# Performance work log

Measured on AMD Instinct MI355X. Metric: run time of the kernel, lower is better.

Reference implementation:

```python
import jax, jax.numpy as jnp
import numpy as np

NUM_HEADS = 12

def _rotate_half(t):
    t1, t2 = jnp.split(t, 2, axis=-1)
    return jnp.concatenate([-t2, t1], axis=-1)

def _rope_apply(t, sin, cos):
    # t: [B,H,N,Dh]; sin/cos: [N,Dh] broadcast over B,H
    return t * cos + _rotate_half(t) * sin


def setup_inputs() -> dict:
    key = jax.random.key(0)
    ks = jax.random.split(key, 6)
    B, N, D = 2, 2048, 768
    Dh = D // NUM_HEADS
    return {
        "x": jax.random.normal(ks[0], (B, N, D), dtype=jnp.float32),
        "sin": jax.random.uniform(ks[1], (N, Dh), dtype=jnp.float32),
        "cos": jax.random.uniform(ks[2], (N, Dh), dtype=jnp.float32),
        "qkv_w": jax.random.normal(ks[3], (3 * D, D), dtype=jnp.float32) * (D ** -0.5),
        "proj_w": jax.random.normal(ks[4], (D, D), dtype=jnp.float32) * (D ** -0.5),
        "proj_b": jax.random.normal(ks[5], (D,), dtype=jnp.float32),
    }


def reference(x, sin, cos, qkv_w, proj_w, proj_b):
    B, N, D = x.shape
    H = NUM_HEADS
    Dh = D // H
    scale = Dh ** -0.5
    # fused QKV projection (qkv_bias=False)
    qkv = jnp.einsum("bnd,ed->bne", x, qkv_w)              # [B,N,3D]
    qkv = qkv.reshape(B, N, 3, H, Dh)
    q = jnp.transpose(qkv[:, :, 0], (0, 2, 1, 3))          # [B,H,N,Dh]
    k = jnp.transpose(qkv[:, :, 1], (0, 2, 1, 3))
    v = jnp.transpose(qkv[:, :, 2], (0, 2, 1, 3))
    # inline RoPE (prefix = 0: sin/cos cover all N positions)
    q = _rope_apply(q, sin, cos)
    k = _rope_apply(k, sin, cos)
    # scaled dot-product attention
    scores = jnp.einsum("bhqd,bhkd->bhqk", q, k) * scale   # [B,H,N,N]
    attn = jax.nn.softmax(scores, axis=-1)
    out = jnp.einsum("bhqk,bhkd->bhqd", attn, v)           # [B,H,N,Dh]
    out = jnp.transpose(out, (0, 2, 1, 3)).reshape(B, N, D)
    # output projection
    return jnp.einsum("bnd,ed->bne", out, proj_w) + proj_b
```

## Files before the change

### kernel.cpp

```cpp
#include <hip/hip_runtime.h>
#include <hip/hip_bf16.h>
#include <stdint.h>


typedef unsigned short u16;
typedef __attribute__((ext_vector_type(8))) short s16x8;
typedef __attribute__((ext_vector_type(4))) short s16x4;
typedef __attribute__((ext_vector_type(4))) float f32x4;

#define MFMA16(a, b, c) __builtin_amdgcn_mfma_f32_16x16x32_bf16((a), (b), (c), 0, 0, 0)

__device__ __forceinline__ f32x4 mfma_k16(s16x4 a, s16x4 b, f32x4 c) {
    asm("s_nop 3\n\tv_mfma_f32_16x16x16_bf16 %0, %1, %2, %0"
        : "+v"(c) : "v"(a), "v"(b));
    return c;
}

__device__ __forceinline__ u16 f2bf(float f) {
    uint32_t u = __float_as_uint(f);
    u = u + 0x7fffu + ((u >> 16) & 1u);
    return (u16)(u >> 16);
}
__device__ __forceinline__ uint32_t pk2(float lo, float hi) {
    return (uint32_t)f2bf(lo) | ((uint32_t)f2bf(hi) << 16);
}
__device__ __forceinline__ uint32_t pk2t(float lo, float hi) {
    return __builtin_amdgcn_perm(__float_as_uint(hi), __float_as_uint(lo),
                                 0x07060302u);
}
__device__ __forceinline__ float fexp2(float x) { return __builtin_amdgcn_exp2f(x); }

__device__ __forceinline__ void gload16(const void* g, void* l) {
    __builtin_amdgcn_global_load_lds(
        (const __attribute__((address_space(1))) unsigned int*)g,
        (__attribute__((address_space(3))) unsigned int*)l,
        16, 0, 0);
}

__global__ __launch_bounds__(256)
void k_cvt3(const float* __restrict__ s0, const float* __restrict__ s1,
            const float* __restrict__ s2, u16* __restrict__ dst,
            int a, int ab, int tot)
{
    const int i = blockIdx.x * 256 + threadIdx.x;
    if (i >= tot) return;
    const float4* src;
    if (i < a)       src = (const float4*)s0 + i;
    else if (i < ab) src = (const float4*)s1 + (i - a);
    else             src = (const float4*)s2 + (i - ab);
    const float4 v = *src;
    ushort4 o;
    o.x = f2bf(v.x); o.y = f2bf(v.y); o.z = f2bf(v.z); o.w = f2bf(v.w);
    ((ushort4*)dst)[i] = o;
}

__global__ __launch_bounds__(256, 2)
void k_qkv_rope(const u16* __restrict__ X,
                const u16* __restrict__ W,
                const float* __restrict__ SIN,
                const float* __restrict__ COS,
                u16* __restrict__ qws, u16* __restrict__ kws, u16* __restrict__ vtws)
{
    __shared__ u16 smem[17408];
    u16* const As0 = smem;
    u16* const Bs0 = smem + 8192;

    const int t  = threadIdx.x;
    const int l  = t & 63;
    const int w  = t >> 6;
    const int cl = l & 15, gh = l >> 4;
    const int brow = blockIdx.x * 128;
    const int bcol = blockIdx.y * 128;
    const int wr = (w >> 1) * 64;
    const int wc = (w & 1) * 64;

    const int srow = w * 16 + (l >> 2);
    const int scol = (((l & 3) ^ ((l >> 3) & 3)) * 8);
    const u16* gA = X + (size_t)(brow + srow) * 768 + scol;
    const u16* gB = W + (size_t)(bcol + srow) * 768 + scol;

    const int csw = ((cl >> 1) & 3);

    f32x4 acc[4][4] = {};

    gload16(gA,            As0 + w * 512);
    gload16(gA + 64 * 768, As0 + 2048 + w * 512);
    gload16(gB,            Bs0 + w * 512);
    gload16(gB + 64 * 768, Bs0 + 2048 + w * 512);
    __syncthreads();

    for (int kt = 0; kt < 24; ++kt) {
        const int cur = kt & 1;
        if (kt + 1 < 24) {
            const int k0 = (kt + 1) * 32;
            u16* An = As0 + (cur ^ 1) * 4096;
            u16* Bn = Bs0 + (cur ^ 1) * 4096;
            gload16(gA + k0,            An + w * 512);
            gload16(gA + k0 + 64 * 768, An + 2048 + w * 512);
            gload16(gB + k0,            Bn + w * 512);
            gload16(gB + k0 + 64 * 768, Bn + 2048 + w * 512);
        }
        const char* Ac = (const char*)(As0 + cur * 4096);
        const char* Bc = (const char*)(Bs0 + cur * 4096);
        s16x8 af[4], bv[4];
        #pragma unroll
        for (int m = 0; m < 4; ++m) {
            const int row = wr + m * 16 + cl;
            af[m] = *(const s16x8*)(Ac + row * 64 + ((gh ^ csw) << 4));
        }
        #pragma unroll
        for (int n = 0; n < 4; ++n) {
            const int row = wc + n * 16 + cl;
            bv[n] = *(const s16x8*)(Bc + row * 64 + ((gh ^ csw) << 4));
        }
        #pragma unroll
        for (int m = 0; m < 4; ++m)
            #pragma unroll
            for (int n = 0; n < 4; ++n)
                acc[m][n] = MFMA16(af[m], bv[n], acc[m][n]);
        __syncthreads();
    }

    if (blockIdx.y >= 12) {
        u16* const Vt = smem;
        #pragma unroll
        for (int m = 0; m < 4; ++m)
            #pragma unroll
            for (int jj = 0; jj < 4; ++jj) {
                const int rowl = wr + m * 16 + gh * 4 + jj;
                #pragma unroll
                for (int n = 0; n < 4; ++n)
                    Vt[(wc + n * 16 + cl) * 136 + rowl] = f2bf(acc[m][n][jj]);
            }
        __syncthreads();
        const int dhcol = t >> 1;
        const int c     = t & 1;
        const int gcol  = bcol + dhcol;
        const int h     = (gcol >> 6) - 24;
        const int dh    = gcol & 63;
        const int b     = brow >> 11;
        const int tok0  = (brow & 2047) + c * 64;
        u16* dst = vtws + ((size_t)(b * 12 + h) * 64 + dh) * 2048 + tok0;
        const uint4* src = (const uint4*)((const char*)Vt + dhcol * 272 + c * 128);
        #pragma unroll
        for (int j = 0; j < 8; ++j)
            ((uint4*)dst)[j] = src[j];
    } else {
        const int seg   = (bcol + wc) >> 6;
        const int which = seg / 12;
        const int h     = seg % 12;
        const float qscl = (which == 0) ? 0.1803368801111244f : 1.0f;
        u16* outp = (which == 0) ? qws : kws;

        #pragma unroll
        for (int m = 0; m < 4; ++m) {
            #pragma unroll
            for (int jj = 0; jj < 4; ++jj) {
                const int row = brow + wr + m * 16 + gh * 4 + jj;
                const int b   = row >> 11;
                const int tok = row & 2047;
                u16* orow = outp + ((size_t)(b * 12 + h) * 2048 + tok) * 64;
                const float* srow2 = SIN + tok * 64;
                const float* crow2 = COS + tok * 64;
                #pragma unroll
                for (int n = 0; n < 4; ++n) {
                    const int dh = n * 16 + cl;
                    const float v = acc[m][n][jj];
                    const float partner = (n < 2) ? -acc[m][n + 2][jj] : acc[m][n - 2][jj];
                    orow[dh] = f2bf((v * crow2[dh] + partner * srow2[dh]) * qscl);
                }
            }
        }
    }
}

__global__ __launch_bounds__(256, 3)
void k_attn(const u16* __restrict__ Qg, const u16* __restrict__ Kg,
            const u16* __restrict__ VTg, u16* __restrict__ Og)
{
    __shared__ u16 Ks[3][64 * 64];
    __shared__ u16 Vs[3][64 * 64];

    const int t  = threadIdx.x;
    const int l  = t & 63;
    const int w  = t >> 6;
    const int cl = l & 15, gh = l >> 4;

    const int i  = blockIdx.x;
    const int bh = (i & 7) * 3 + ((i >> 3) % 3);
    const int qt = i / 24;
    const int qb = qt * 64;

    const u16* Q  = Qg  + (size_t)bh * 2048 * 64;
    const char* Kb  = (const char*)(Kg  + (size_t)bh * 2048 * 64);
    const char* VTb = (const char*)(VTg + (size_t)bh * 64 * 2048);

    s16x8 qf[4][2];
    #pragma unroll
    for (int m = 0; m < 4; ++m)
        #pragma unroll
        for (int ks = 0; ks < 2; ++ks)
            qf[m][ks] = *(const s16x8*)(Q + (((qb + m * 16 + cl) << 6) + ks * 32 + gh * 8));

    f32x4 o[4][4] = {};
    float lrun[4] = {};

    const int srow8 = l >> 3;
    const int scolb = (((l & 7) ^ srow8) << 4);
    const int rsw = (cl & 7) << 4;

#define STAGE(T, KB, VB)                                                      \
    {                                                                         \
        const int nb_ = (T) * 64;                                             \
        _Pragma("unroll")                                                     \
        for (int c = 0; c < 2; ++c) {                                         \
            const int s = c * 4 + w;                                          \
            const int grow = s * 8 + srow8;                                   \
            gload16(Kb  + (nb_ + grow) * 128 + scolb,    &(KB)[s * 512]);     \
            gload16(VTb + grow * 4096 + nb_ * 2 + scolb, &(VB)[s * 512]);     \
        }                                                                     \
    }

    STAGE(0, Ks[0], Vs[0])
    STAGE(1, Ks[1], Vs[1])
    asm volatile("s_waitcnt vmcnt(4)" ::: "memory");
    __builtin_amdgcn_s_barrier();

    int ci = 0;
    for (int kt = 0; kt < 32; ++kt) {
        if (kt + 2 < 32) {
            const int ii = (ci + 2 >= 3) ? ci - 1 : ci + 2;
            STAGE(kt + 2, Ks[ii], Vs[ii])
        }

        const char* kl = (const char*)Ks[ci];
        const char* vl = (const char*)Vs[ci];
        s16x8 kf[2];
        s16x4 vf[4];
        #pragma unroll
        for (int ks = 0; ks < 2; ++ks)
            kf[ks] = *(const s16x8*)(kl + (w * 16 + cl) * 128 + ((ks * 64 + gh * 16) ^ rsw));
        #pragma unroll
        for (int n = 0; n < 4; ++n)
            vf[n] = *(const s16x4*)(vl + (n * 16 + cl) * 128 + ((w * 32 + gh * 8) ^ rsw));

        f32x4 st[4];
        #pragma unroll
        for (int m = 0; m < 4; ++m)
            #pragma unroll
            for (int jj = 0; jj < 4; ++jj)
                st[m][jj] = -12.f;
        #pragma unroll
        for (int m = 0; m < 4; ++m)
            #pragma unroll
            for (int ks = 0; ks < 2; ++ks)
                st[m] = MFMA16(kf[ks], qf[m][ks], st[m]);

        union { uint32_t u[2]; s16x4 v; } pd[4];
        #pragma unroll
        for (int m = 0; m < 4; ++m) {
            const float p0 = fexp2(st[m][0]);
            const float p1 = fexp2(st[m][1]);
            const float p2 = fexp2(st[m][2]);
            const float p3 = fexp2(st[m][3]);
            lrun[m] += (p0 + p1) + (p2 + p3);
            pd[m].u[0] = pk2t(p0, p1);
            pd[m].u[1] = pk2t(p2, p3);
        }

        #pragma unroll
        for (int n = 0; n < 4; ++n)
            #pragma unroll
            for (int m = 0; m < 4; ++m)
                o[n][m] = mfma_k16(vf[n], pd[m].v, o[n][m]);

        if (kt < 30) asm volatile("s_waitcnt vmcnt(4)" ::: "memory");
        else         asm volatile("s_waitcnt vmcnt(0)" ::: "memory");
        __builtin_amdgcn_s_barrier();

        ci = (ci == 2) ? 0 : ci + 1;
    }
#undef STAGE

    f32x4* OL = (f32x4*)&Ks[0][0];
    float*  ML = (float*)&Vs[0][0];
    const int b = bh / 12, h = bh % 12;

    #pragma unroll
    for (int m = 0; m < 4; ++m) {
        float lr = lrun[m];
        lr += __shfl_xor(lr, 16);
        lr += __shfl_xor(lr, 32);
        ML[(m * 4 + w) * 64 + l] = lr;
    }

    #pragma unroll
    for (int m = 0; m < 4; ++m) {
        __syncthreads();
        #pragma unroll
        for (int n = 0; n < 4; ++n)
            OL[(n * 4 + w) * 64 + l] = o[n][m];
        __syncthreads();
        f32x4 oacc = OL[(w * 4 + 0) * 64 + l];
        oacc += OL[(w * 4 + 1) * 64 + l];
        oacc += OL[(w * 4 + 2) * 64 + l];
        oacc += OL[(w * 4 + 3) * 64 + l];
        const float lt = ML[(m * 4 + 0) * 64 + l] + ML[(m * 4 + 1) * 64 + l]
                       + ML[(m * 4 + 2) * 64 + l] + ML[(m * 4 + 3) * 64 + l];
        const float inv = 1.0f / lt;
        const int tok = qb + m * 16 + cl;
        u16* orow = Og + ((size_t)(b * 2048 + tok)) * 768 + h * 64 + w * 16 + gh * 4;
        uint2 pkv;
        pkv.x = pk2(oacc[0] * inv, oacc[1] * inv);
        pkv.y = pk2(oacc[2] * inv, oacc[3] * inv);
        *(uint2*)orow = pkv;
    }
}

__global__ __launch_bounds__(256, 2)
void k_proj(const u16* __restrict__ A,
            const u16* __restrict__ W,
            const float* __restrict__ BIAS,
            float* __restrict__ OUT)
{
    __shared__ u16 smem[16384];
    u16* const As0 = smem;
    u16* const Bs0 = smem + 8192;

    const int t  = threadIdx.x;
    const int l  = t & 63;
    const int w  = t >> 6;
    const int cl = l & 15, gh = l >> 4;
    const int brow = blockIdx.x * 128;
    const int bcol = blockIdx.y * 128;
    const int wr = (w >> 1) * 64;
    const int wc = (w & 1) * 64;

    const int srow = w * 16 + (l >> 2);
    const int scol = (((l & 3) ^ ((l >> 3) & 3)) * 8);
    const u16* gA = A + (size_t)(brow + srow) * 768 + scol;
    const u16* gB = W + (size_t)(bcol + srow) * 768 + scol;
    const int csw = ((cl >> 1) & 3);

    f32x4 acc[4][4] = {};

    gload16(gA,            As0 + w * 512);
    gload16(gA + 64 * 768, As0 + 2048 + w * 512);
    gload16(gB,            Bs0 + w * 512);
    gload16(gB + 64 * 768, Bs0 + 2048 + w * 512);
    __syncthreads();

    for (int kt = 0; kt < 24; ++kt) {
        const int cur = kt & 1;
        if (kt + 1 < 24) {
            const int k0 = (kt + 1) * 32;
            u16* An = As0 + (cur ^ 1) * 4096;
            u16* Bn = Bs0 + (cur ^ 1) * 4096;
            gload16(gA + k0,            An + w * 512);
            gload16(gA + k0 + 64 * 768, An + 2048 + w * 512);
            gload16(gB + k0,            Bn + w * 512);
            gload16(gB + k0 + 64 * 768, Bn + 2048 + w * 512);
        }
        const char* Ac = (const char*)(As0 + cur * 4096);
        const char* Bc = (const char*)(Bs0 + cur * 4096);
        s16x8 af[4], bv[4];
        #pragma unroll
        for (int m = 0; m < 4; ++m) {
            const int row = wr + m * 16 + cl;
            af[m] = *(const s16x8*)(Ac + row * 64 + ((gh ^ csw) << 4));
        }
        #pragma unroll
        for (int n = 0; n < 4; ++n) {
            const int row = wc + n * 16 + cl;
            bv[n] = *(const s16x8*)(Bc + row * 64 + ((gh ^ csw) << 4));
        }
        #pragma unroll
        for (int m = 0; m < 4; ++m)
            #pragma unroll
            for (int n = 0; n < 4; ++n)
                acc[m][n] = MFMA16(af[m], bv[n], acc[m][n]);
        __syncthreads();
    }

    #pragma unroll
    for (int m = 0; m < 4; ++m) {
        #pragma unroll
        for (int jj = 0; jj < 4; ++jj) {
            const int row = brow + wr + m * 16 + gh * 4 + jj;
            #pragma unroll
            for (int n = 0; n < 4; ++n) {
                const int col = bcol + wc + n * 16 + cl;
                OUT[(size_t)row * 768 + col] = acc[m][n][jj] + BIAS[col];
            }
        }
    }
}

extern "C" void kernel_launch(void* const* d_in, const int* in_sizes, int n_in,
                              void* d_out, int out_size, void* d_ws, size_t ws_size,
                              hipStream_t stream)
{
    const float* x     = (const float*)d_in[0];
    const float* sinp  = (const float*)d_in[1];
    const float* cosp  = (const float*)d_in[2];
    const float* qkv_w = (const float*)d_in[3];
    const float* projw = (const float*)d_in[4];
    const float* projb = (const float*)d_in[5];
    float* out = (float*)d_out;

    const size_t N_X  = (size_t)4096 * 768;
    const size_t N_WQ = (size_t)2304 * 768;
    const size_t N_WP = (size_t)768 * 768;
    const size_t SEG  = (size_t)2 * 12 * 2048 * 64;

    u16* xbf   = (u16*)d_ws;
    u16* wqkv  = xbf + N_X;
    u16* wproj = wqkv + N_WQ;
    u16* qws   = wproj + N_WP;
    u16* kws   = qws + SEG;
    u16* vtws  = kws + SEG;
    u16* aws   = vtws + SEG;

    const int a   = (int)(N_X / 4);
    const int ab  = (int)((N_X + N_WQ) / 4);
    const int tot = (int)((N_X + N_WQ + N_WP) / 4);
    k_cvt3<<<(tot + 255) / 256, 256, 0, stream>>>(x, qkv_w, projw, xbf, a, ab, tot);

    k_qkv_rope<<<dim3(32, 18), 256, 0, stream>>>(xbf, wqkv, sinp, cosp, qws, kws, vtws);
    k_attn    <<<768, 256, 0, stream>>>(qws, kws, vtws, aws);
    k_proj    <<<dim3(32, 6),  256, 0, stream>>>(aws, wproj, projb, out);
}
```

Before: 93.23 us.

## Stage Q/K RoPE epilogue through LDS for vectorized stores; batch PV MFMAs in one asm

The QKV GEMM epilogue for Q and K now writes bf16 accumulators into shared memory. Each thread then reads one contiguous 64-wide head row, applies RoPE with vectorized sin/cos loads, and writes 16-byte stores. Before, every lane did scattered 2-byte stores and scalar sin/cos loads. Separately, the 16 PV MFMAs in attention are issued from one asm block with a single s_nop instead of one nop per instruction. RoPE now runs on bf16-rounded values, which adds a rounding step, and the single asm block removes the compiler's freedom to schedule around those MFMAs.

```diff
diff --git a/kernel.cpp b/kernel.cpp
--- a/kernel.cpp
+++ b/kernel.cpp
@@ -10,16 +10,13 @@
 
 #define MFMA16(a, b, c) __builtin_amdgcn_mfma_f32_16x16x32_bf16((a), (b), (c), 0, 0, 0)
 
-__device__ __forceinline__ f32x4 mfma_k16(s16x4 a, s16x4 b, f32x4 c) {
-    asm("s_nop 3\n\tv_mfma_f32_16x16x16_bf16 %0, %1, %2, %0"
-        : "+v"(c) : "v"(a), "v"(b));
-    return c;
-}
-
 __device__ __forceinline__ u16 f2bf(float f) {
     uint32_t u = __float_as_uint(f);
     u = u + 0x7fffu + ((u >> 16) & 1u);
     return (u16)(u >> 16);
+}
+__device__ __forceinline__ float bf2f(u16 u) {
+    return __uint_as_float(((uint32_t)u) << 16);
 }
 __device__ __forceinline__ uint32_t pk2(float lo, float hi) {
     return (uint32_t)f2bf(lo) | ((uint32_t)f2bf(hi) << 16);
@@ -146,30 +143,62 @@
         for (int j = 0; j < 8; ++j)
             ((uint4*)dst)[j] = src[j];
     } else {
-        const int seg   = (bcol + wc) >> 6;
+        u16* const T = smem;
+        #pragma unroll
+        for (int m = 0; m < 4; ++m)
+            #pragma unroll
+            for (int jj = 0; jj < 4; ++jj) {
+                const int rowl = wr + m * 16 + gh * 4 + jj;
+                #pragma unroll
+                for (int n = 0; n < 4; ++n)
+                    T[rowl * 136 + wc + n * 16 + cl] = f2bf(acc[m][n][jj]);
+            }
+        __syncthreads();
+        const int r   = t >> 1;
+        const int c   = t & 1;
+        const int row = brow + r;
+        const int b   = row >> 11;
+        const int tok = row & 2047;
+        const int seg = (bcol >> 6) + c;
         const int which = seg / 12;
         const int h     = seg % 12;
         const float qscl = (which == 0) ? 0.1803368801111244f : 1.0f;
-        u16* outp = (which == 0) ? qws : kws;
-
-        #pragma unroll
-        for (int m = 0; m < 4; ++m) {
-            #pragma unroll
-            for (int jj = 0; jj < 4; ++jj) {
-                const int row = brow + wr + m * 16 + gh * 4 + jj;
-                const int b   = row >> 11;
-                const int tok = row & 2047;
-                u16* orow = outp + ((size_t)(b * 12 + h) * 2048 + tok) * 64;
-                const float* srow2 = SIN + tok * 64;
-                const float* crow2 = COS + tok * 64;
-                #pragma unroll
-                for (int n = 0; n < 4; ++n) {
-                    const int dh = n * 16 + cl;
-                    const float v = acc[m][n][jj];
-                    const float partner = (n < 2) ? -acc[m][n + 2][jj] : acc[m][n - 2][jj];
-                    orow[dh] = f2bf((v * crow2[dh] + partner * srow2[dh]) * qscl);
-                }
+        u16* orow = ((which == 0) ? qws : kws) + ((size_t)(b * 12 + h) * 2048 + tok) * 64;
+        const float* sn = SIN + tok * 64;
+        const float* cs = COS + tok * 64;
+        const u16* Trow = T + r * 136 + c * 64;
+
+        #pragma unroll
+        for (int j = 0; j < 4; ++j) {
+            const s16x8 lo = *(const s16x8*)(Trow + j * 8);
+            const s16x8 hi = *(const s16x8*)(Trow + 32 + j * 8);
+            float csl[8], csh[8], snl[8], snh[8];
+            *(float4*)&csl[0] = *(const float4*)(cs + j * 8);
+            *(float4*)&csl[4] = *(const float4*)(cs + j * 8 + 4);
+            *(float4*)&csh[0] = *(const float4*)(cs + 32 + j * 8);
+            *(float4*)&csh[4] = *(const float4*)(cs + 32 + j * 8 + 4);
+            *(float4*)&snl[0] = *(const float4*)(sn + j * 8);
+            *(float4*)&snl[4] = *(const float4*)(sn + j * 8 + 4);
+            *(float4*)&snh[0] = *(const float4*)(sn + 32 + j * 8);
+            *(float4*)&snh[4] = *(const float4*)(sn + 32 + j * 8 + 4);
+            float vl[8], vh[8];
+            #pragma unroll
+            for (int e = 0; e < 8; ++e) {
+                vl[e] = bf2f((u16)lo[e]);
+                vh[e] = bf2f((u16)hi[e]);
             }
+            uint32_t ol[4], oh[4];
+            #pragma unroll
+            for (int e = 0; e < 4; ++e) {
+                const float a0 = (vl[2*e]   * csl[2*e]   - vh[2*e]   * snl[2*e])   * qscl;
+                const float a1 = (vl[2*e+1] * csl[2*e+1] - vh[2*e+1] * snl[2*e+1]) * qscl;
+                const float b0 = (vh[2*e]   * csh[2*e]   + vl[2*e]   * snh[2*e])   * qscl;
+                const float b1 = (vh[2*e+1] * csh[2*e+1] + vl[2*e+1] * snh[2*e+1]) * qscl;
+                ol[e] = pk2(a0, a1);
+                oh[e] = pk2(b0, b1);
+            }
+            *(uint4*)(orow + j * 8)      = make_uint4(ol[0], ol[1], ol[2], ol[3]);
+            *(uint4*)(orow + 32 + j * 8) = make_uint4(oh[0], oh[1], oh[2], oh[3]);
         }
     }
 }
@@ -268,11 +297,30 @@
             pd[m].u[1] = pk2t(p2, p3);
         }
 
-        #pragma unroll
-        for (int n = 0; n < 4; ++n)
-            #pragma unroll
-            for (int m = 0; m < 4; ++m)
-                o[n][m] = mfma_k16(vf[n], pd[m].v, o[n][m]);
+        asm volatile(
+            "s_nop 3\n\t"
+            "v_mfma_f32_16x16x16_bf16 %0, %16, %20, %0\n\t"
+            "v_mfma_f32_16x16x16_bf16 %1, %16, %21, %1\n\t"
+            "v_mfma_f32_16x16x16_bf16 %2, %16, %22, %2\n\t"
+            "v_mfma_f32_16x16x16_bf16 %3, %16, %23, %3\n\t"
+            "v_mfma_f32_16x16x16_bf16 %4, %17, %20, %4\n\t"
+            "v_mfma_f32_16x16x16_bf16 %5, %17, %21, %5\n\t"
+            "v_mfma_f32_16x16x16_bf16 %6, %17, %22, %6\n\t"
+            "v_mfma_f32_16x16x16_bf16 %7, %17, %23, %7\n\t"
+            "v_mfma_f32_16x16x16_bf16 %8, %18, %20, %8\n\t"
+            "v_mfma_f32_16x16x16_bf16 %9, %18, %21, %9\n\t"
+            "v_mfma_f32_16x16x16_bf16 %10, %18, %22, %10\n\t"
+            "v_mfma_f32_16x16x16_bf16 %11, %18, %23, %11\n\t"
+            "v_mfma_f32_16x16x16_bf16 %12, %19, %20, %12\n\t"
+            "v_mfma_f32_16x16x16_bf16 %13, %19, %21, %13\n\t"
+            "v_mfma_f32_16x16x16_bf16 %14, %19, %22, %14\n\t"
+            "v_mfma_f32_16x16x16_bf16 %15, %19, %23, %15"
+            : "+v"(o[0][0]), "+v"(o[0][1]), "+v"(o[0][2]), "+v"(o[0][3]),
+              "+v"(o[1][0]), "+v"(o[1][1]), "+v"(o[1][2]), "+v"(o[1][3]),
+              "+v"(o[2][0]), "+v"(o[2][1]), "+v"(o[2][2]), "+v"(o[2][3]),
+              "+v"(o[3][0]), "+v"(o[3][1]), "+v"(o[3][2]), "+v"(o[3][3])
+            : "v"(vf[0]), "v"(vf[1]), "v"(vf[2]), "v"(vf[3]),
+              "v"(pd[0].v), "v"(pd[1].v), "v"(pd[2].v), "v"(pd[3].v));
 
         if (kt < 30) asm volatile("s_waitcnt vmcnt(4)" ::: "memory");
         else         asm volatile("s_waitcnt vmcnt(0)" ::: "memory");
```

After: 104.2 us. 1.12x slower.
